# Performance work log

Measured on AMD Instinct MI355X. Metric: run time of the kernel, lower is better.

## Reference

```python
import jax, jax.numpy as jnp
import numpy as np

B_, J_, D_, E_, N_, K_ = 32, 1024, 192, 384, 16, 3


def _dwconv(x, w, b):
    # x: (B,J,E), w: (E,1,K) depthwise, b: (E,)
    xc = jnp.transpose(x, (0, 2, 1))  # (B,E,J)
    pad = w.shape[2] // 2
    y = jax.lax.conv_general_dilated(
        xc, w, window_strides=(1,), padding=[(pad, pad)],
        feature_group_count=w.shape[0], dimension_numbers=('NCH', 'OIH', 'NCH'))
    return jnp.transpose(y + b[None, :, None], (0, 2, 1))  # (B,J,E)


def _scan_dir(x, cw, cb, WB, bB, WC, bC, WD, bD, A, Wi, bi, Wr, br):
    # One directional selective-SSM pass. x: (B,J,E); A: (N,) negative diag.
    xc = _dwconv(x, cw, cb)                       # (B,J,E)
    Bt = xc @ WB + bB                             # (B,J,N)
    Ct = xc @ WC + bC                             # (B,J,N)
    Dt = jax.nn.softplus(xc @ WD + bD)            # Delta, (B,J,N)
    A_bar = jnp.exp(Dt * A)                       # ZOH discretization
    B_bar = (A_bar - 1.0) / (A + 1e-6) * Bt
    u = xc @ Wi + bi                              # in_to_state, (B,J,N)
    Bu = B_bar * u

    def step(h, ab_bu):
        ab, bu = ab_bu
        h = ab * h + bu
        return h, h

    h0 = jnp.zeros((x.shape[0], A.shape[0]), x.dtype)
    _, hs = jax.lax.scan(step, h0, (jnp.swapaxes(A_bar, 0, 1), jnp.swapaxes(Bu, 0, 1)))
    hs = jnp.swapaxes(hs, 0, 1)                   # (B,J,N)
    return (hs * Ct) @ Wr + br                    # readout, (B,J,E)


def setup_inputs() -> dict:
    key = jax.random.key(0)
    ks = iter(jax.random.split(key, 40))

    def nrm(shape, scale=0.02):
        return jax.random.normal(next(ks), shape, jnp.float32) * scale

    inp = {
        'tokens': jax.random.normal(next(ks), (B_, J_, D_), jnp.float32),
        'norm_g': jnp.ones((D_,), jnp.float32),
        'norm_b': jnp.zeros((D_,), jnp.float32),
        'Wx': nrm((D_, E_)), 'bx': jnp.zeros((E_,), jnp.float32),
        'Wz': nrm((D_, E_)), 'bz': jnp.zeros((E_,), jnp.float32),
        'convf_w': nrm((E_, 1, K_), 0.1), 'convf_b': jnp.zeros((E_,), jnp.float32),
        'convb_w': nrm((E_, 1, K_), 0.1), 'convb_b': jnp.zeros((E_,), jnp.float32),
        'WBf': nrm((E_, N_)), 'bBf': jnp.zeros((N_,), jnp.float32),
        'WCf': nrm((E_, N_)), 'bCf': jnp.zeros((N_,), jnp.float32),
        'WDf': nrm((E_, N_)), 'bDf': jnp.zeros((N_,), jnp.float32),
        'WBb': nrm((E_, N_)), 'bBb': jnp.zeros((N_,), jnp.float32),
        'WCb': nrm((E_, N_)), 'bCb': jnp.zeros((N_,), jnp.float32),
        'WDb': nrm((E_, N_)), 'bDb': jnp.zeros((N_,), jnp.float32),
        'A_log': nrm((N_,), 0.5),
        'Wi': nrm((E_, N_)), 'bi': jnp.zeros((N_,), jnp.float32),
        'Wr': nrm((N_, E_)), 'br': jnp.zeros((E_,), jnp.float32),
        'Wo': nrm((E_, D_)), 'bo': jnp.zeros((D_,), jnp.float32),
    }
    return inp


def reference(tokens, norm_g, norm_b, Wx, bx, Wz, bz, convf_w, convf_b,
              convb_w, convb_b, WBf, bBf, WCf, bCf, WDf, bDf, WBb, bBb,
              WCb, bCb, WDb, bDb, A_log, Wi, bi, Wr, br, Wo, bo):
    # LayerNorm (biased variance, eps=1e-5, like torch)
    mu = jnp.mean(tokens, axis=-1, keepdims=True)
    var = jnp.mean(jnp.square(tokens - mu), axis=-1, keepdims=True)
    t = (tokens - mu) / jnp.sqrt(var + 1e-5) * norm_g + norm_b

    x = t @ Wx + bx
    z = t @ Wz + bz
    gate = jax.nn.sigmoid(jax.nn.silu(z))

    # A computed under no_grad in torch -> stop_gradient here
    A = jax.lax.stop_gradient(-jax.nn.softplus(A_log))

    y_f = _scan_dir(x, convf_w, convf_b, WBf, bBf, WCf, bCf, WDf, bDf, A, Wi, bi, Wr, br)
    y_b = jnp.flip(_scan_dir(jnp.flip(x, 1), convb_w, convb_b, WBb, bBb, WCb, bCb,
                             WDb, bDb, A, Wi, bi, Wr, br), 1)
    y = (y_f + y_b) * gate
    return tokens + y @ Wo + bo
```

## Files before the change

kernel.cpp:

```cpp
#include <hip/hip_runtime.h>
#include <math.h>


typedef __attribute__((ext_vector_type(8))) short short8;
typedef __attribute__((ext_vector_type(4))) float f32x4;

__device__ __forceinline__ unsigned short f2bf(float f){
  union { float f; unsigned u; } v; v.f = f;
  unsigned r = v.u + 0x7FFFu + ((v.u >> 16) & 1u);
  return (unsigned short)(r >> 16);
}
__device__ __forceinline__ float bf2f(unsigned short s){
  union { unsigned u; float f; } v; v.u = ((unsigned)s) << 16;
  return v.f;
}
__device__ __forceinline__ float softplusf(float x){
  return (x > 20.f) ? x : log1pf(expf(x));
}
__device__ __forceinline__ float softplus_fast(float x){
  return (x > 20.f) ? x : __logf(1.f + __expf(x));
}
__device__ __forceinline__ float sigf_fast(float x){
  return __builtin_amdgcn_rcpf(1.f + __expf(-x));
}

__global__ __launch_bounds__(256) void prep_kernel(
    const float* __restrict__ Wx, const float* __restrict__ Wz,
    const float* __restrict__ WBf, const float* __restrict__ WCf,
    const float* __restrict__ WDf, const float* __restrict__ WBb,
    const float* __restrict__ WCb, const float* __restrict__ WDb,
    const float* __restrict__ Wi, const float* __restrict__ Wr,
    const float* __restrict__ Wo,
    const float* __restrict__ bBf, const float* __restrict__ bCf,
    const float* __restrict__ bDf, const float* __restrict__ bBb,
    const float* __restrict__ bCb, const float* __restrict__ bDb,
    const float* __restrict__ bi,
    unsigned short* __restrict__ Wxz_t, unsigned short* __restrict__ W4f_t,
    unsigned short* __restrict__ W4b_t, unsigned short* __restrict__ Wrt2,
    unsigned short* __restrict__ Wot, float* __restrict__ b4f,
    float* __restrict__ b4b)
{
  int idx = blockIdx.x * 256 + threadIdx.x;
  if (idx < 147456){ int n = idx / 192, k = idx % 192;
    Wxz_t[idx] = f2bf(n < 384 ? Wx[k*384 + n] : Wz[k*384 + n - 384]); return; }
  idx -= 147456;
  if (idx < 24576){ int n = idx / 384, k = idx % 384;
    const float* W = (n<16)?WBf:(n<32)?WCf:(n<48)?WDf:Wi;
    W4f_t[idx] = f2bf(W[k*16 + (n&15)]); return; }
  idx -= 24576;
  if (idx < 24576){ int n = idx / 384, k = idx % 384;
    const float* W = (n<16)?WBb:(n<32)?WCb:(n<48)?WDb:Wi;
    W4b_t[idx] = f2bf(W[k*16 + (n&15)]); return; }
  idx -= 24576;
  if (idx < 12288){ int n = idx / 32, k = idx % 32;
    Wrt2[idx] = f2bf(Wr[(k&15)*384 + n]); return; }
  idx -= 12288;
  if (idx < 73728){ int n = idx / 384, k = idx % 384;
    Wot[idx] = f2bf(Wo[k*192 + n]); return; }
  idx -= 73728;
  if (idx < 64){
    const float* bsel = (idx<16)?bBf:(idx<32)?bCf:(idx<48)?bDf:bi;
    b4f[idx] = bsel[idx & 15]; return; }
  idx -= 64;
  if (idx < 64){
    const float* bsel = (idx<16)?bBb:(idx<32)?bCb:(idx<48)?bDb:bi;
    b4b[idx] = bsel[idx & 15]; return; }
}

__global__ __launch_bounds__(256) void ln_kernel(
    const float* __restrict__ tokens, const float* __restrict__ g,
    const float* __restrict__ nb, unsigned short* __restrict__ t_bf)
{
  __shared__ unsigned short s[32 * 200];
  const int t = threadIdx.x;
  const int bid = blockIdx.x;
  const int a = bid >> 4, x = bid & 7, h = (bid >> 3) & 1;
  const int v = a*8 + x;
  const int row0 = (v*2 + h) * 32;
  {
    const int r = t >> 3, l8 = t & 7;
    const float* tr = tokens + (long)(row0 + r) * 192;
    float vv[24], sm = 0.f, sq = 0.f;
#pragma unroll
    for (int i = 0; i < 24; i++){ float xx = tr[l8 + 8*i]; vv[i] = xx; sm += xx; sq += xx*xx; }
#pragma unroll
    for (int m = 1; m < 8; m <<= 1){ sm += __shfl_xor(sm, m); sq += __shfl_xor(sq, m); }
    const float mu = sm * (1.f/192.f);
    const float rstd = rsqrtf(sq * (1.f/192.f) - mu*mu + 1e-5f);
#pragma unroll
    for (int i = 0; i < 24; i++){
      const int d = l8 + 8*i;
      s[r*200 + d] = f2bf((vv[i] - mu)*rstd*g[d] + nb[d]);
    }
  }
  __syncthreads();
  {
#pragma unroll
    for (int i = 0; i < 3; i++){
      const int item = i*256 + t;
      const int row = item / 24, c8 = item % 24;
      *(short8*)&t_bf[(long)(row0 + row)*192 + c8*8] =
          *(const short8*)&s[row*200 + c8*8];
    }
  }
}

__global__ __launch_bounds__(256) void xz_gemm(
    const unsigned short* __restrict__ t_bf,
    const unsigned short* __restrict__ Wxz_t,
    const float* __restrict__ bx, const float* __restrict__ bz,
    unsigned short* __restrict__ x_bf, unsigned short* __restrict__ gate_bf)
{
  __shared__ unsigned short tl[64 * 200];
  const int t = threadIdx.x;
  const int bid = blockIdx.x;
  const int a = bid / 48, rem = bid % 48;
  const int ct = rem >> 3;
  const int rt = a*8 + (rem & 7);
  const int row0 = rt * 64;

  {
#pragma unroll
    for (int i = 0; i < 6; i++){
      const int item = i*256 + t;
      const int row = item / 24, c8 = item % 24;
      *(short8*)&tl[row*200 + c8*8] =
          *(const short8*)&t_bf[(long)(row0 + row)*192 + c8*8];
    }
  }
  __syncthreads();

  const int lane = t & 63, w = t >> 6;
  const int l15 = lane & 15, q = lane >> 4;
  const int C0 = ct*128 + w*32;

  f32x4 acc[4][2];
#pragma unroll
  for (int m = 0; m < 4; m++)
#pragma unroll
    for (int nf = 0; nf < 2; nf++) acc[m][nf] = (f32x4){0.f,0.f,0.f,0.f};

  const unsigned short* wb = Wxz_t + (long)(C0 + l15)*192 + q*8;
#pragma unroll
  for (int ks = 0; ks < 6; ks++){
    const int k0 = ks * 32;
    short8 a0 = *(const short8*)&tl[(     l15)*200 + k0 + q*8];
    short8 a1 = *(const short8*)&tl[(16 + l15)*200 + k0 + q*8];
    short8 a2 = *(const short8*)&tl[(32 + l15)*200 + k0 + q*8];
    short8 a3 = *(const short8*)&tl[(48 + l15)*200 + k0 + q*8];
#pragma unroll
    for (int nf = 0; nf < 2; nf++){
      short8 bw = *(const short8*)&wb[nf*16*192 + k0];
      acc[0][nf] = __builtin_amdgcn_mfma_f32_16x16x32_bf16(a0, bw, acc[0][nf], 0, 0, 0);
      acc[1][nf] = __builtin_amdgcn_mfma_f32_16x16x32_bf16(a1, bw, acc[1][nf], 0, 0, 0);
      acc[2][nf] = __builtin_amdgcn_mfma_f32_16x16x32_bf16(a2, bw, acc[2][nf], 0, 0, 0);
      acc[3][nf] = __builtin_amdgcn_mfma_f32_16x16x32_bf16(a3, bw, acc[3][nf], 0, 0, 0);
    }
  }
  __syncthreads();

  unsigned short* stg = tl;
  const int isgate = (ct >= 3);
#pragma unroll
  for (int nf = 0; nf < 2; nf++){
    const int c = C0 + nf*16 + l15;
    const float bv = isgate ? bz[c - 384] : bx[c];
#pragma unroll
    for (int m = 0; m < 4; m++){
#pragma unroll
      for (int r = 0; r < 4; r++){
        float val = acc[m][nf][r] + bv;
        if (isgate){ const float si = val * sigf_fast(val); val = sigf_fast(si); }
        stg[(m*16 + q*4 + r)*136 + (w*32 + nf*16 + l15)] = f2bf(val);
      }
    }
  }
  __syncthreads();

  {
    unsigned short* outp = isgate ? gate_bf : x_bf;
    const int cb = isgate ? (ct*128 - 384) : (ct*128);
#pragma unroll
    for (int i = 0; i < 4; i++){
      const int item = i*256 + t;
      const int row = item / 16, c8 = item % 16;
      *(short8*)&outp[(long)(row0 + row)*384 + cb + c8*8] =
          *(const short8*)&stg[row*136 + c8*8];
    }
  }
}

__global__ __launch_bounds__(256) void proj_mfma(
    const unsigned short* __restrict__ x_bf,
    const float* __restrict__ cwf, const float* __restrict__ cbf,
    const float* __restrict__ cwb, const float* __restrict__ cbb,
    const unsigned short* __restrict__ W4f, const unsigned short* __restrict__ W4b,
    const float* __restrict__ b4f, const float* __restrict__ b4b,
    const float* __restrict__ A_log,
    float* __restrict__ Af, float* __restrict__ Buf, float* __restrict__ Ctf,
    float* __restrict__ Ab, float* __restrict__ Bub, float* __restrict__ Ctb)
{
  __shared__ unsigned short xc[32 * 392];
  float* pj = (float*)xc;
  const int t = threadIdx.x;
  const int bid = blockIdx.x;
  const int dir = bid >> 10;
  const int r10 = bid & 1023;
  const int av = r10 >> 4, xv = r10 & 7, hv = (r10 >> 3) & 1;
  const int v = av*8 + xv;
  const int u = v*2 + hv;
  const int b = u >> 5;
  const int jt = dir ? (31 - (u & 31)) : (u & 31);
  const int j0 = jt * 32;
  const float* cw = dir ? cwb : cwf;
  const float* cb = dir ? cbb : cbf;
  const unsigned short* W4 = dir ? W4b : W4f;
  const float* b4 = dir ? b4b : b4f;
  float* Aout = dir ? Ab  : Af;
  float* Bout = dir ? Bub : Buf;
  float* Cout = dir ? Ctb : Ctf;

  {
    const long xrow = (long)b * 1024 * 384;
#pragma unroll
    for (int i = 0; i < 6; i++){
      const int idx = i*256 + t;
      const int r = idx / 48;
      const int e0 = (idx - r*48) * 8;
      const int jp = j0 + r;
      short8 xm = (short8){0,0,0,0,0,0,0,0};
      short8 xp = (short8){0,0,0,0,0,0,0,0};
      if (jp >= 1){
        const int js = dir ? 1024 - jp : jp - 1;
        xm = *(const short8*)&x_bf[xrow + (long)js*384 + e0];
      }
      short8 x0;
      {
        const int js = dir ? 1023 - jp : jp;
        x0 = *(const short8*)&x_bf[xrow + (long)js*384 + e0];
      }
      if (jp <= 1022){
        const int js = dir ? 1022 - jp : jp + 1;
        xp = *(const short8*)&x_bf[xrow + (long)js*384 + e0];
      }
      float wv[24], cbv[8];
#pragma unroll
      for (int vv = 0; vv < 6; vv++)
        *(float4*)&wv[vv*4] = *(const float4*)&cw[e0*3 + vv*4];
#pragma unroll
      for (int vv = 0; vv < 2; vv++)
        *(float4*)&cbv[vv*4] = *(const float4*)&cb[e0 + vv*4];
      short8 o;
#pragma unroll
      for (int m = 0; m < 8; m++){
        const float acc = fmaf(wv[3*m],   bf2f((unsigned short)xm[m]),
                          fmaf(wv[3*m+1], bf2f((unsigned short)x0[m]),
                          fmaf(wv[3*m+2], bf2f((unsigned short)xp[m]), cbv[m])));
        o[m] = (short)f2bf(acc);
      }
      *(short8*)&xc[r*392 + e0] = o;
    }
  }
  __syncthreads();

  const int lane = t & 63, w = t >> 6;
  const int l15 = lane & 15, q = lane >> 4;
  const int rt = w & 1, ng = w >> 1;
  f32x4 acc[2];
#pragma unroll
  for (int nf = 0; nf < 2; nf++) acc[nf] = (f32x4){0.f,0.f,0.f,0.f};
  const unsigned short* wb = W4 + (long)(ng*32 + l15)*384 + q*8;
#pragma unroll
  for (int ks = 0; ks < 12; ks++){
    const int k0 = ks * 32;
    short8 a = *(const short8*)&xc[(rt*16 + l15)*392 + k0 + q*8];
#pragma unroll
    for (int nf = 0; nf < 2; nf++){
      short8 bw = *(const short8*)&wb[nf*16*384 + k0];
      acc[nf] = __builtin_amdgcn_mfma_f32_16x16x32_bf16(a, bw, acc[nf], 0, 0, 0);
    }
  }
  __syncthreads();

  {
#pragma unroll
    for (int nf = 0; nf < 2; nf++){
      const int col = ng*32 + nf*16 + l15;
#pragma unroll
      for (int r = 0; r < 4; r++)
        pj[col*34 + rt*16 + q*4 + r] = acc[nf][r];
    }
  }
  __syncthreads();

  {
#pragma unroll
    for (int i = 0; i < 2; i++){
      const int idx = i*256 + t;
      const int n = idx >> 5, j = idx & 31;
      const float Bt  = pj[(     n)*34 + j] + b4[n];
      const float Ctv = pj[(16 + n)*34 + j] + b4[16 + n];
      const float dt  = softplus_fast(pj[(32 + n)*34 + j] + b4[32 + n]);
      const float u2  = pj[(48 + n)*34 + j] + b4[48 + n];
      const float Av  = -softplusf(A_log[n]);
      const float ab  = __expf(dt * Av);
      const float bu  = (ab - 1.f) * __builtin_amdgcn_rcpf(Av + 1e-6f) * Bt * u2;
      const int jp = j0 + j;
      const long base = ((long)b*16 + n) * 1024;
      Aout[base + jp] = ab;
      Bout[base + jp] = bu;
      Cout[base + (dir ? 1023 - jp : jp)] = Ctv;
    }
  }
}

__global__ __launch_bounds__(256) void scan2_kernel(
    const float* __restrict__ Af, const float* __restrict__ Buf, float* __restrict__ hsf,
    const float* __restrict__ Ab, const float* __restrict__ Bub, float* __restrict__ hsb)
{
  __shared__ float sA[256], sB[256];
  const int sel = blockIdx.x >> 9;
  const long base = (long)(blockIdx.x & 511) * 1024;
  const float* Abar = sel ? Ab  : Af;
  const float* Bu   = sel ? Bub : Buf;
  float* hs         = sel ? hsb : hsf;
  const int t = threadIdx.x;
  const float4 a4 = *reinterpret_cast<const float4*>(&Abar[base + t*4]);
  const float4 b4 = *reinterpret_cast<const float4*>(&Bu[base + t*4]);
  float A = a4.x, Bc = b4.x;
  Bc = fmaf(a4.y, Bc, b4.y); A *= a4.y;
  Bc = fmaf(a4.z, Bc, b4.z); A *= a4.z;
  Bc = fmaf(a4.w, Bc, b4.w); A *= a4.w;
  sA[t] = A; sB[t] = Bc;
  __syncthreads();
  for (int off = 1; off < 256; off <<= 1){
    const float cA = sA[t], cB = sB[t];
    float pA = 1.f, pB = 0.f;
    if (t >= off){ pA = sA[t - off]; pB = sB[t - off]; }
    __syncthreads();
    sA[t] = pA * cA;
    sB[t] = fmaf(cA, pB, cB);
    __syncthreads();
  }
  float h = (t > 0) ? sB[t - 1] : 0.f;
  float4 o;
  h = fmaf(a4.x, h, b4.x); o.x = h;
  h = fmaf(a4.y, h, b4.y); o.y = h;
  h = fmaf(a4.z, h, b4.z); o.z = h;
  h = fmaf(a4.w, h, b4.w); o.w = h;
  *reinterpret_cast<float4*>(&hs[base + t*4]) = o;
}

__global__ __launch_bounds__(256) void final_mfma(
    const float* __restrict__ tokens, const unsigned short* __restrict__ gate_bf,
    const float* __restrict__ hsf, const float* __restrict__ Ctf,
    const float* __restrict__ hsb, const float* __restrict__ Ctb,
    const unsigned short* __restrict__ Wrt2, const float* __restrict__ br,
    const unsigned short* __restrict__ Wot, const float* __restrict__ bo,
    float* __restrict__ out)
{
  __shared__ unsigned short s2[16 * 36];
  __shared__ float stgf[16 * 200];
  unsigned short* yg = (unsigned short*)stgf;
  const int t = threadIdx.x;
  const int bid = blockIdx.x;
  const int a = bid >> 5, x = bid & 7, p = (bid >> 3) & 3;
  const int v = a*8 + x;
  const int u16 = v*4 + p;
  const int b  = u16 >> 6;
  const int j0 = (u16 & 63) * 16;

  {
#pragma unroll
    for (int i = 0; i < 2; i++){
      const int idx = i*256 + t;
      const int j = idx & 15, kk = idx >> 4;
      float val;
      if (kk < 16){
        const long pp = ((long)b*16 + kk)*1024 + j0 + j;
        val = hsf[pp] * Ctf[pp];
      } else {
        const long basen = ((long)b*16 + (kk - 16)) * 1024;
        val = hsb[basen + 1023 - (j0 + j)] * Ctb[basen + j0 + j];
      }
      s2[j*36 + kk] = f2bf(val);
    }
  }
  __syncthreads();

  const int lane = t & 63, w = t >> 6;
  const int l15 = lane & 15, q = lane >> 4;

  {
    short8 a1 = *(const short8*)&s2[l15*36 + q*8];
    const unsigned short* wbp = Wrt2 + (long)l15*32 + q*8;
#pragma unroll
    for (int i = 0; i < 6; i++){
      const int nf = w*6 + i;
      short8 bw = *(const short8*)&wbp[nf*16*32];
      f32x4 acc = (f32x4){0.f,0.f,0.f,0.f};
      acc = __builtin_amdgcn_mfma_f32_16x16x32_bf16(a1, bw, acc, 0, 0, 0);
      const int c = nf*16 + l15;
      const float brv = 2.f * br[c];
#pragma unroll
      for (int r = 0; r < 4; r++)
        yg[(q*4 + r)*388 + c] = f2bf(acc[r] + brv);
    }
  }
  __syncthreads();

  {
#pragma unroll
    for (int i = 0; i < 3; i++){
      const int item = i*256 + t;
      const int row = item / 48;
      const int cb  = (item % 48) * 8;
      short8 y8 = *(const short8*)&yg[row*388 + cb];
      short8 g8 = *(const short8*)&gate_bf[((long)b*1024 + j0 + row)*384 + cb];
      short8 o;
#pragma unroll
      for (int m = 0; m < 8; m++)
        o[m] = (short)f2bf(bf2f((unsigned short)y8[m]) * bf2f((unsigned short)g8[m]));
      *(short8*)&yg[row*388 + cb] = o;
    }
  }
  __syncthreads();

  f32x4 acc[3];
  {
#pragma unroll
    for (int i = 0; i < 3; i++) acc[i] = (f32x4){0.f,0.f,0.f,0.f};
    const unsigned short* wbp = Wot + (long)l15*384 + q*8;
#pragma unroll
    for (int ks = 0; ks < 12; ks++){
      const int k0 = ks * 32;
      short8 a2 = *(const short8*)&yg[l15*388 + k0 + q*8];
#pragma unroll
      for (int i = 0; i < 3; i++){
        const int nf = w*3 + i;
        short8 bw = *(const short8*)&wbp[(long)nf*16*384 + k0];
        acc[i] = __builtin_amdgcn_mfma_f32_16x16x32_bf16(a2, bw, acc[i], 0, 0, 0);
      }
    }
  }
  __syncthreads();

  {
    const int gq = q ^ (q >> 1);
#pragma unroll
    for (int i = 0; i < 3; i++){
      const int nf = w*3 + i;
      const int c = nf*16 + l15;
      const float bv = bo[c];
      const int scol = ((nf + gq) % 12)*16 + l15;
#pragma unroll
      for (int r = 0; r < 4; r++)
        stgf[(q*4 + r)*200 + scol] = acc[i][r] + bv;
    }
  }
  __syncthreads();

  {
#pragma unroll
    for (int i = 0; i < 3; i++){
      const int item = i*256 + t;
      const int row = item / 48;
      const int c4  = (item % 48) * 4;
      const int qq = (row >> 2) & 3;
      const int gg = qq ^ (qq >> 1);
      const int nf = c4 / 16;
      const int scol = ((nf + gg) % 12)*16 + (c4 % 16);
      float4 vv = *(const float4*)&stgf[row*200 + scol];
      const long R = (long)b*1024 + j0 + row;
      const float4 tk = *(const float4*)&tokens[R*192 + c4];
      vv.x += tk.x; vv.y += tk.y; vv.z += tk.z; vv.w += tk.w;
      *(float4*)&out[R*192 + c4] = vv;
    }
  }
}

extern "C" void kernel_launch(void* const* d_in, const int* in_sizes, int n_in,
                              void* d_out, int out_size, void* d_ws, size_t ws_size,
                              hipStream_t stream)
{
  const float* tokens  = (const float*)d_in[0];
  const float* norm_g  = (const float*)d_in[1];
  const float* norm_b  = (const float*)d_in[2];
  const float* Wx      = (const float*)d_in[3];
  const float* bx      = (const float*)d_in[4];
  const float* Wz      = (const float*)d_in[5];
  const float* bz      = (const float*)d_in[6];
  const float* convf_w = (const float*)d_in[7];
  const float* convf_b = (const float*)d_in[8];
  const float* convb_w = (const float*)d_in[9];
  const float* convb_b = (const float*)d_in[10];
  const float* WBf     = (const float*)d_in[11];
  const float* bBf     = (const float*)d_in[12];
  const float* WCf     = (const float*)d_in[13];
  const float* bCf     = (const float*)d_in[14];
  const float* WDf     = (const float*)d_in[15];
  const float* bDf     = (const float*)d_in[16];
  const float* WBb     = (const float*)d_in[17];
  const float* bBb     = (const float*)d_in[18];
  const float* WCb     = (const float*)d_in[19];
  const float* bCb     = (const float*)d_in[20];
  const float* WDb     = (const float*)d_in[21];
  const float* bDb     = (const float*)d_in[22];
  const float* A_log   = (const float*)d_in[23];
  const float* Wi      = (const float*)d_in[24];
  const float* bi      = (const float*)d_in[25];
  const float* Wr      = (const float*)d_in[26];
  const float* br      = (const float*)d_in[27];
  const float* Wo      = (const float*)d_in[28];
  const float* bo      = (const float*)d_in[29];

  char* ws = (char*)d_ws;
  unsigned short* x_bf    = (unsigned short*)(ws + 0);
  unsigned short* gate_bf = (unsigned short*)(ws + 25165824);
  unsigned short* Wxz_t   = (unsigned short*)(ws + 50331648);
  unsigned short* W4f_t   = (unsigned short*)(ws + 50626560);
  unsigned short* W4b_t   = (unsigned short*)(ws + 50675712);
  unsigned short* Wrt2    = (unsigned short*)(ws + 50724864);
  unsigned short* Wot     = (unsigned short*)(ws + 50749440);
  float* b4f = (float*)(ws + 50896896);
  float* b4b = (float*)(ws + 50897152);
  float* Af  = (float*)(ws + 50897408);
  float* Buf = (float*)(ws + 52994560);
  float* Ctf = (float*)(ws + 55091712);
  float* hsf = (float*)(ws + 57188864);
  float* Ab  = (float*)(ws + 59286016);
  float* Bub = (float*)(ws + 61383168);
  float* Ctb = (float*)(ws + 63480320);
  float* hsb = (float*)(ws + 65577472);
  unsigned short* t_bf = (unsigned short*)(ws + 67674624);

  prep_kernel<<<1105, 256, 0, stream>>>(Wx, Wz, WBf, WCf, WDf, WBb, WCb, WDb,
                                        Wi, Wr, Wo, bBf, bCf, bDf, bBb, bCb, bDb, bi,
                                        Wxz_t, W4f_t, W4b_t, Wrt2, Wot, b4f, b4b);
  ln_kernel<<<1024, 256, 0, stream>>>(tokens, norm_g, norm_b, t_bf);
  xz_gemm<<<3072, 256, 0, stream>>>(t_bf, Wxz_t, bx, bz, x_bf, gate_bf);
  proj_mfma<<<2048, 256, 0, stream>>>(x_bf, convf_w, convf_b, convb_w, convb_b,
                                      W4f_t, W4b_t, b4f, b4b, A_log,
                                      Af, Buf, Ctf, Ab, Bub, Ctb);
  scan2_kernel<<<1024, 256, 0, stream>>>(Af, Buf, hsf, Ab, Bub, hsb);
  final_mfma<<<2048, 256, 0, stream>>>(tokens, gate_bf, hsf, Ctf, hsb, Ctb,
                                       Wrt2, br, Wot, bo, (float*)d_out);
}
```

Measured before the change: 133.1 us.

## Split final fused kernel into readout GEMM and output GEMM with 32-row tiles

Result: slower. 142.3 us (+6.9%).

```diff
diff --git a/kernel.cpp b/kernel.cpp
--- a/kernel.cpp
+++ b/kernel.cpp
@@ -351,52 +351,51 @@
   *reinterpret_cast<float4*>(&hs[base + t*4]) = o;
 }
 
-__global__ __launch_bounds__(256) void final_mfma(
-    const float* __restrict__ tokens, const unsigned short* __restrict__ gate_bf,
+__global__ __launch_bounds__(256) void yr_gemm(
     const float* __restrict__ hsf, const float* __restrict__ Ctf,
     const float* __restrict__ hsb, const float* __restrict__ Ctb,
+    const unsigned short* __restrict__ gate_bf,
     const unsigned short* __restrict__ Wrt2, const float* __restrict__ br,
-    const unsigned short* __restrict__ Wot, const float* __restrict__ bo,
-    float* __restrict__ out)
-{
-  __shared__ unsigned short s2[16 * 36];
-  __shared__ float stgf[16 * 200];
-  unsigned short* yg = (unsigned short*)stgf;
+    unsigned short* __restrict__ yg_g)
+{
+  __shared__ unsigned short s2[32 * 40];
+  __shared__ unsigned short yg[32 * 392];
   const int t = threadIdx.x;
   const int bid = blockIdx.x;
-  const int a = bid >> 5, x = bid & 7, p = (bid >> 3) & 3;
-  const int v = a*8 + x;
-  const int u16 = v*4 + p;
-  const int b  = u16 >> 6;
-  const int j0 = (u16 & 63) * 16;
-
-  {
-#pragma unroll
-    for (int i = 0; i < 2; i++){
+  const int av = bid >> 4, xv = bid & 7, hv = (bid >> 3) & 1;
+  const int v = av*8 + xv;
+  const int u = v*2 + hv;
+  const int b  = u >> 5;
+  const int j0 = (u & 31) * 32;
+
+  {
+#pragma unroll
+    for (int i = 0; i < 4; i++){
       const int idx = i*256 + t;
-      const int j = idx & 15, kk = idx >> 4;
+      const int j = idx & 31, kk = idx >> 5;
       float val;
       if (kk < 16){
-        const long pp = ((long)b*16 + kk)*1024 + j0 + j;
-        val = hsf[pp] * Ctf[pp];
+        const long p = ((long)b*16 + kk)*1024 + j0 + j;
+        val = hsf[p] * Ctf[p];
       } else {
         const long basen = ((long)b*16 + (kk - 16)) * 1024;
         val = hsb[basen + 1023 - (j0 + j)] * Ctb[basen + j0 + j];
       }
-      s2[j*36 + kk] = f2bf(val);
+      s2[j*40 + kk] = f2bf(val);
     }
   }
   __syncthreads();
 
   const int lane = t & 63, w = t >> 6;
   const int l15 = lane & 15, q = lane >> 4;
-
-  {
-    short8 a1 = *(const short8*)&s2[l15*36 + q*8];
+  const int rt = w & 1, ng = w >> 1;
+
+  {
+    short8 a1 = *(const short8*)&s2[(rt*16 + l15)*40 + q*8];
     const unsigned short* wbp = Wrt2 + (long)l15*32 + q*8;
 #pragma unroll
-    for (int i = 0; i < 6; i++){
-      const int nf = w*6 + i;
+    for (int i = 0; i < 12; i++){
+      const int nf = ng*12 + i;
       short8 bw = *(const short8*)&wbp[nf*16*32];
       f32x4 acc = (f32x4){0.f,0.f,0.f,0.f};
       acc = __builtin_amdgcn_mfma_f32_16x16x32_bf16(a1, bw, acc, 0, 0, 0);
@@ -404,42 +403,71 @@
       const float brv = 2.f * br[c];
 #pragma unroll
       for (int r = 0; r < 4; r++)
-        yg[(q*4 + r)*388 + c] = f2bf(acc[r] + brv);
-    }
-  }
-  __syncthreads();
-
-  {
-#pragma unroll
-    for (int i = 0; i < 3; i++){
+        yg[(rt*16 + q*4 + r)*392 + c] = f2bf(acc[r] + brv);
+    }
+  }
+  __syncthreads();
+
+  {
+#pragma unroll
+    for (int i = 0; i < 6; i++){
       const int item = i*256 + t;
       const int row = item / 48;
       const int cb  = (item % 48) * 8;
-      short8 y8 = *(const short8*)&yg[row*388 + cb];
+      short8 y8 = *(const short8*)&yg[row*392 + cb];
       short8 g8 = *(const short8*)&gate_bf[((long)b*1024 + j0 + row)*384 + cb];
       short8 o;
 #pragma unroll
       for (int m = 0; m < 8; m++)
         o[m] = (short)f2bf(bf2f((unsigned short)y8[m]) * bf2f((unsigned short)g8[m]));
-      *(short8*)&yg[row*388 + cb] = o;
-    }
-  }
-  __syncthreads();
-
-  f32x4 acc[3];
-  {
-#pragma unroll
-    for (int i = 0; i < 3; i++) acc[i] = (f32x4){0.f,0.f,0.f,0.f};
-    const unsigned short* wbp = Wot + (long)l15*384 + q*8;
+      *(short8*)&yg_g[((long)b*1024 + j0 + row)*384 + cb] = o;
+    }
+  }
+}
+
+__global__ __launch_bounds__(256) void out_gemm(
+    const unsigned short* __restrict__ yg_g,
+    const unsigned short* __restrict__ Wot, const float* __restrict__ bo,
+    const float* __restrict__ tokens, float* __restrict__ out)
+{
+  __shared__ float stgf[32 * 204];
+  unsigned short* yt = (unsigned short*)stgf;
+  const int t = threadIdx.x;
+  const int bid = blockIdx.x;
+  const int av = bid >> 4, xv = bid & 7, hv = (bid >> 3) & 1;
+  const int v = av*8 + xv;
+  const int u = v*2 + hv;
+  const int b  = u >> 5;
+  const int j0 = (u & 31) * 32;
+
+  {
+#pragma unroll
+    for (int i = 0; i < 6; i++){
+      const int item = i*256 + t;
+      const int row = item / 48, c8 = item % 48;
+      *(short8*)&yt[row*408 + c8*8] =
+          *(const short8*)&yg_g[((long)b*1024 + j0 + row)*384 + c8*8];
+    }
+  }
+  __syncthreads();
+
+  const int lane = t & 63, w = t >> 6;
+  const int l15 = lane & 15, q = lane >> 4;
+  const int rt = w & 1, cg = w >> 1;
+
+  f32x4 acc[6];
+#pragma unroll
+  for (int i = 0; i < 6; i++) acc[i] = (f32x4){0.f,0.f,0.f,0.f};
+  {
+    const unsigned short* wbp = Wot + (long)(cg*96 + l15)*384 + q*8;
 #pragma unroll
     for (int ks = 0; ks < 12; ks++){
       const int k0 = ks * 32;
-      short8 a2 = *(const short8*)&yg[l15*388 + k0 + q*8];
-#pragma unroll
-      for (int i = 0; i < 3; i++){
-        const int nf = w*3 + i;
-        short8 bw = *(const short8*)&wbp[(long)nf*16*384 + k0];
-        acc[i] = __builtin_amdgcn_mfma_f32_16x16x32_bf16(a2, bw, acc[i], 0, 0, 0);
+      short8 a = *(const short8*)&yt[(rt*16 + l15)*408 + k0 + q*8];
+#pragma unroll
+      for (int i = 0; i < 6; i++){
+        short8 bw = *(const short8*)&wbp[(long)i*16*384 + k0];
+        acc[i] = __builtin_amdgcn_mfma_f32_16x16x32_bf16(a, bw, acc[i], 0, 0, 0);
       }
     }
   }
@@ -448,21 +476,21 @@
   {
     const int gq = q ^ (q >> 1);
 #pragma unroll
-    for (int i = 0; i < 3; i++){
-      const int nf = w*3 + i;
+    for (int i = 0; i < 6; i++){
+      const int nf = cg*6 + i;
       const int c = nf*16 + l15;
       const float bv = bo[c];
       const int scol = ((nf + gq) % 12)*16 + l15;
 #pragma unroll
       for (int r = 0; r < 4; r++)
-        stgf[(q*4 + r)*200 + scol] = acc[i][r] + bv;
-    }
-  }
-  __syncthreads();
-
-  {
-#pragma unroll
-    for (int i = 0; i < 3; i++){
+        stgf[(rt*16 + q*4 + r)*204 + scol] = acc[i][r] + bv;
+    }
+  }
+  __syncthreads();
+
+  {
+#pragma unroll
+    for (int i = 0; i < 6; i++){
       const int item = i*256 + t;
       const int row = item / 48;
       const int c4  = (item % 48) * 4;
@@ -470,7 +498,7 @@
       const int gg = qq ^ (qq >> 1);
       const int nf = c4 / 16;
       const int scol = ((nf + gg) % 12)*16 + (c4 % 16);
-      float4 vv = *(const float4*)&stgf[row*200 + scol];
+      float4 vv = *(const float4*)&stgf[row*204 + scol];
       const long R = (long)b*1024 + j0 + row;
       const float4 tk = *(const float4*)&tokens[R*192 + c4];
       vv.x += tk.x; vv.y += tk.y; vv.z += tk.z; vv.w += tk.w;
@@ -533,6 +561,7 @@
   float* Ctb = (float*)(ws + 63480320);
   float* hsb = (float*)(ws + 65577472);
   unsigned short* t_bf = (unsigned short*)(ws + 67674624);
+  unsigned short* yg_g = x_bf;
 
   prep_kernel<<<1105, 256, 0, stream>>>(Wx, Wz, WBf, WCf, WDf, WBb, WCb, WDb,
                                         Wi, Wr, Wo, bBf, bCf, bDf, bBb, bCb, bDb, bi,
@@ -543,6 +572,6 @@
                                       W4f_t, W4b_t, b4f, b4b, A_log,
                                       Af, Buf, Ctf, Ab, Bub, Ctb);
   scan2_kernel<<<1024, 256, 0, stream>>>(Af, Buf, hsf, Ab, Bub, hsb);
-  final_mfma<<<2048, 256, 0, stream>>>(tokens, gate_bf, hsf, Ctf, hsb, Ctb,
-                                       Wrt2, br, Wot, bo, (float*)d_out);
-}
+  yr_gemm<<<1024, 256, 0, stream>>>(hsf, Ctf, hsb, Ctb, gate_bf, Wrt2, br, yg_g);
+  out_gemm<<<1024, 256, 0, stream>>>(yg_g, Wot, bo, tokens, (float*)d_out);
+}
```

## Fuse forward and backward direction projections into one block sharing x loads

Applied to the files above, without the earlier changes.

Result: no change. 132.3 us (-0.6%).

```diff
diff --git a/kernel.cpp b/kernel.cpp
--- a/kernel.cpp
+++ b/kernel.cpp
@@ -200,25 +200,18 @@
     float* __restrict__ Af, float* __restrict__ Buf, float* __restrict__ Ctf,
     float* __restrict__ Ab, float* __restrict__ Bub, float* __restrict__ Ctb)
 {
-  __shared__ unsigned short xc[32 * 392];
-  float* pj = (float*)xc;
+  __shared__ unsigned short xcf[32 * 392];
+  __shared__ unsigned short xcb[32 * 392];
+  float* pjf = (float*)xcf;
+  float* pjb = (float*)xcb;
   const int t = threadIdx.x;
   const int bid = blockIdx.x;
-  const int dir = bid >> 10;
-  const int r10 = bid & 1023;
-  const int av = r10 >> 4, xv = r10 & 7, hv = (r10 >> 3) & 1;
+  const int av = bid >> 4, xv = bid & 7, hv = (bid >> 3) & 1;
   const int v = av*8 + xv;
   const int u = v*2 + hv;
-  const int b = u >> 5;
-  const int jt = dir ? (31 - (u & 31)) : (u & 31);
-  const int j0 = jt * 32;
-  const float* cw = dir ? cwb : cwf;
-  const float* cb = dir ? cbb : cbf;
-  const unsigned short* W4 = dir ? W4b : W4f;
-  const float* b4 = dir ? b4b : b4f;
-  float* Aout = dir ? Ab  : Af;
-  float* Bout = dir ? Bub : Buf;
-  float* Cout = dir ? Ctb : Ctf;
+  const int b  = u >> 5;
+  const int j0 = (u & 31) * 32;
+  const int jb0 = 992 - j0;
 
   {
     const long xrow = (long)b * 1024 * 384;
@@ -230,35 +223,49 @@
       const int jp = j0 + r;
       short8 xm = (short8){0,0,0,0,0,0,0,0};
       short8 xp = (short8){0,0,0,0,0,0,0,0};
-      if (jp >= 1){
-        const int js = dir ? 1024 - jp : jp - 1;
-        xm = *(const short8*)&x_bf[xrow + (long)js*384 + e0];
-      }
-      short8 x0;
+      if (jp >= 1)    xm = *(const short8*)&x_bf[xrow + (long)(jp-1)*384 + e0];
+      short8 x0      = *(const short8*)&x_bf[xrow + (long)jp*384 + e0];
+      if (jp <= 1022) xp = *(const short8*)&x_bf[xrow + (long)(jp+1)*384 + e0];
+
+      float xmf[8], x0f[8], xpf[8];
+#pragma unroll
+      for (int m = 0; m < 8; m++){
+        xmf[m] = bf2f((unsigned short)xm[m]);
+        x0f[m] = bf2f((unsigned short)x0[m]);
+        xpf[m] = bf2f((unsigned short)xp[m]);
+      }
       {
-        const int js = dir ? 1023 - jp : jp;
-        x0 = *(const short8*)&x_bf[xrow + (long)js*384 + e0];
-      }
-      if (jp <= 1022){
-        const int js = dir ? 1022 - jp : jp + 1;
-        xp = *(const short8*)&x_bf[xrow + (long)js*384 + e0];
-      }
-      float wv[24], cbv[8];
-#pragma unroll
-      for (int vv = 0; vv < 6; vv++)
-        *(float4*)&wv[vv*4] = *(const float4*)&cw[e0*3 + vv*4];
-#pragma unroll
-      for (int vv = 0; vv < 2; vv++)
-        *(float4*)&cbv[vv*4] = *(const float4*)&cb[e0 + vv*4];
-      short8 o;
-#pragma unroll
-      for (int m = 0; m < 8; m++){
-        const float acc = fmaf(wv[3*m],   bf2f((unsigned short)xm[m]),
-                          fmaf(wv[3*m+1], bf2f((unsigned short)x0[m]),
-                          fmaf(wv[3*m+2], bf2f((unsigned short)xp[m]), cbv[m])));
-        o[m] = (short)f2bf(acc);
-      }
-      *(short8*)&xc[r*392 + e0] = o;
+        float wv[24], cbv[8];
+#pragma unroll
+        for (int vv = 0; vv < 6; vv++)
+          *(float4*)&wv[vv*4] = *(const float4*)&cwf[e0*3 + vv*4];
+#pragma unroll
+        for (int vv = 0; vv < 2; vv++)
+          *(float4*)&cbv[vv*4] = *(const float4*)&cbf[e0 + vv*4];
+        short8 o;
+#pragma unroll
+        for (int m = 0; m < 8; m++)
+          o[m] = (short)f2bf(fmaf(wv[3*m], xmf[m],
+                            fmaf(wv[3*m+1], x0f[m],
+                            fmaf(wv[3*m+2], xpf[m], cbv[m]))));
+        *(short8*)&xcf[r*392 + e0] = o;
+      }
+      {
+        float wv[24], cbv[8];
+#pragma unroll
+        for (int vv = 0; vv < 6; vv++)
+          *(float4*)&wv[vv*4] = *(const float4*)&cwb[e0*3 + vv*4];
+#pragma unroll
+        for (int vv = 0; vv < 2; vv++)
+          *(float4*)&cbv[vv*4] = *(const float4*)&cbb[e0 + vv*4];
+        short8 o;
+#pragma unroll
+        for (int m = 0; m < 8; m++)
+          o[m] = (short)f2bf(fmaf(wv[3*m], xpf[m],
+                            fmaf(wv[3*m+1], x0f[m],
+                            fmaf(wv[3*m+2], xmf[m], cbv[m]))));
+        *(short8*)&xcb[(31 - r)*392 + e0] = o;
+      }
     }
   }
   __syncthreads();
@@ -266,18 +273,23 @@
   const int lane = t & 63, w = t >> 6;
   const int l15 = lane & 15, q = lane >> 4;
   const int rt = w & 1, ng = w >> 1;
-  f32x4 acc[2];
-#pragma unroll
-  for (int nf = 0; nf < 2; nf++) acc[nf] = (f32x4){0.f,0.f,0.f,0.f};
-  const unsigned short* wb = W4 + (long)(ng*32 + l15)*384 + q*8;
+  f32x4 accF[2], accB[2];
+#pragma unroll
+  for (int nf = 0; nf < 2; nf++){ accF[nf] = (f32x4){0.f,0.f,0.f,0.f};
+                                  accB[nf] = (f32x4){0.f,0.f,0.f,0.f}; }
+  const unsigned short* wbF = W4f + (long)(ng*32 + l15)*384 + q*8;
+  const unsigned short* wbB = W4b + (long)(ng*32 + l15)*384 + q*8;
 #pragma unroll
   for (int ks = 0; ks < 12; ks++){
     const int k0 = ks * 32;
-    short8 a = *(const short8*)&xc[(rt*16 + l15)*392 + k0 + q*8];
+    short8 aF = *(const short8*)&xcf[(rt*16 + l15)*392 + k0 + q*8];
+    short8 aB = *(const short8*)&xcb[(rt*16 + l15)*392 + k0 + q*8];
 #pragma unroll
     for (int nf = 0; nf < 2; nf++){
-      short8 bw = *(const short8*)&wb[nf*16*384 + k0];
-      acc[nf] = __builtin_amdgcn_mfma_f32_16x16x32_bf16(a, bw, acc[nf], 0, 0, 0);
+      short8 bwF = *(const short8*)&wbF[nf*16*384 + k0];
+      short8 bwB = *(const short8*)&wbB[nf*16*384 + k0];
+      accF[nf] = __builtin_amdgcn_mfma_f32_16x16x32_bf16(aF, bwF, accF[nf], 0, 0, 0);
+      accB[nf] = __builtin_amdgcn_mfma_f32_16x16x32_bf16(aB, bwB, accB[nf], 0, 0, 0);
     }
   }
   __syncthreads();
@@ -287,8 +299,10 @@
     for (int nf = 0; nf < 2; nf++){
       const int col = ng*32 + nf*16 + l15;
 #pragma unroll
-      for (int r = 0; r < 4; r++)
-        pj[col*34 + rt*16 + q*4 + r] = acc[nf][r];
+      for (int r = 0; r < 4; r++){
+        pjf[col*34 + rt*16 + q*4 + r] = accF[nf][r];
+        pjb[col*34 + rt*16 + q*4 + r] = accB[nf][r];
+      }
     }
   }
   __syncthreads();
@@ -298,18 +312,29 @@
     for (int i = 0; i < 2; i++){
       const int idx = i*256 + t;
       const int n = idx >> 5, j = idx & 31;
-      const float Bt  = pj[(     n)*34 + j] + b4[n];
-      const float Ctv = pj[(16 + n)*34 + j] + b4[16 + n];
-      const float dt  = softplus_fast(pj[(32 + n)*34 + j] + b4[32 + n]);
-      const float u2  = pj[(48 + n)*34 + j] + b4[48 + n];
       const float Av  = -softplusf(A_log[n]);
-      const float ab  = __expf(dt * Av);
-      const float bu  = (ab - 1.f) * __builtin_amdgcn_rcpf(Av + 1e-6f) * Bt * u2;
-      const int jp = j0 + j;
+      const float rAv = __builtin_amdgcn_rcpf(Av + 1e-6f);
       const long base = ((long)b*16 + n) * 1024;
-      Aout[base + jp] = ab;
-      Bout[base + jp] = bu;
-      Cout[base + (dir ? 1023 - jp : jp)] = Ctv;
+      {
+        const float Bt  = pjf[(     n)*34 + j] + b4f[n];
+        const float Ctv = pjf[(16 + n)*34 + j] + b4f[16 + n];
+        const float dt  = softplus_fast(pjf[(32 + n)*34 + j] + b4f[32 + n]);
+        const float u2  = pjf[(48 + n)*34 + j] + b4f[48 + n];
+        const float ab  = __expf(dt * Av);
+        Af [base + j0 + j] = ab;
+        Buf[base + j0 + j] = (ab - 1.f) * rAv * Bt * u2;
+        Ctf[base + j0 + j] = Ctv;
+      }
+      {
+        const float Bt  = pjb[(     n)*34 + j] + b4b[n];
+        const float Ctv = pjb[(16 + n)*34 + j] + b4b[16 + n];
+        const float dt  = softplus_fast(pjb[(32 + n)*34 + j] + b4b[32 + n]);
+        const float u2  = pjb[(48 + n)*34 + j] + b4b[48 + n];
+        const float ab  = __expf(dt * Av);
+        Ab [base + jb0 + j] = ab;
+        Bub[base + jb0 + j] = (ab - 1.f) * rAv * Bt * u2;
+        Ctb[base + 1023 - (jb0 + j)] = Ctv;
+      }
     }
   }
 }
@@ -539,7 +564,7 @@
                                         Wxz_t, W4f_t, W4b_t, Wrt2, Wot, b4f, b4b);
   ln_kernel<<<1024, 256, 0, stream>>>(tokens, norm_g, norm_b, t_bf);
   xz_gemm<<<3072, 256, 0, stream>>>(t_bf, Wxz_t, bx, bz, x_bf, gate_bf);
-  proj_mfma<<<2048, 256, 0, stream>>>(x_bf, convf_w, convf_b, convb_w, convb_b,
+  proj_mfma<<<1024, 256, 0, stream>>>(x_bf, convf_w, convf_b, convb_w, convb_b,
                                       W4f_t, W4b_t, b4f, b4b, A_log,
                                       Af, Buf, Ctf, Ab, Bub, Ctb);
   scan2_kernel<<<1024, 256, 0, stream>>>(Af, Buf, hsf, Ab, Bub, hsb);
```
